# Kernel tuning notes

Hardware: AMD Instinct MI355X
Metric: run time of the kernel (lower is better)

The kernel has to match this reference:

```python
import jax, jax.numpy as jnp
import numpy as np

L, B, T, D = 4, 2, 1024, 2048
HQ, HKV, DK = 16, 4, 128
HID = 5464
CAND = 896


def setup_inputs() -> dict:
    key = jax.random.key(0)
    ks = jax.random.split(key, 8)
    s = lambda fan: fan ** -0.5
    return {
        "x": jax.random.normal(ks[0], (B, T, D), jnp.float32),
        "s1": jnp.ones((L, D), jnp.float32),
        "s2": jnp.ones((L, D), jnp.float32),
        "s3": jnp.ones((L, D), jnp.float32),
        "wq": jax.random.normal(ks[1], (L, D, HQ * DK), jnp.float32) * s(D),
        "wk": jax.random.normal(ks[2], (L, D, HKV * DK), jnp.float32) * s(D),
        "wv": jax.random.normal(ks[3], (L, D, HKV * DK), jnp.float32) * s(D),
        "wo": jax.random.normal(ks[4], (L, HQ * DK, D), jnp.float32) * s(HQ * DK),
        "w_gate": jax.random.normal(ks[5], (L, D, HID), jnp.float32) * s(D),
        "w_val": jax.random.normal(ks[6], (L, D, HID), jnp.float32) * s(D),
        "w_out": jax.random.normal(ks[7], (L, HID, D), jnp.float32) * s(HID),
        "cand_offset": CAND,
    }


def _rmsnorm(x, scale, eps=1e-5):
    xf = x.astype(jnp.float32)
    n = xf * jax.lax.rsqrt(jnp.mean(xf * xf, axis=-1, keepdims=True) + eps)
    return (scale * n).astype(x.dtype)


def _rope_cos_sin(t_len, dk):
    inv = 1.0 / (10000.0 ** (jnp.arange(0, dk, 2, dtype=jnp.float32) / dk))
    fr = jnp.outer(jnp.arange(t_len, dtype=jnp.float32), inv)
    emb = jnp.concatenate([fr, fr], axis=-1)  # [T, dk]
    return jnp.cos(emb)[None, :, None, :], jnp.sin(emb)[None, :, None, :]


def _rotate_half(x):
    x1, x2 = jnp.split(x, 2, axis=-1)
    return jnp.concatenate([-x2, x1], axis=-1)


def reference(x, s1, s2, s3, wq, wk, wv, wo, w_gate, w_val, w_out, cand_offset):
    Bsz, Tlen, _ = x.shape
    # recsys mask: causal history; candidates attend to history + self only
    r = jnp.arange(Tlen)[:, None]
    c = jnp.arange(Tlen)[None, :]
    mask = (c <= r) & ~((r >= cand_offset) & (c >= cand_offset) & (r != c))  # [T,T] bool
    cos, sin = _rope_cos_sin(Tlen, DK)
    nrep = HQ // HKV
    h = x
    for l in range(wq.shape[0]):
        hn = _rmsnorm(h, s1[l])
        q = (hn @ wq[l]).reshape(Bsz, Tlen, HQ, DK)
        k = (hn @ wk[l]).reshape(Bsz, Tlen, HKV, DK)
        v = (hn @ wv[l]).reshape(Bsz, Tlen, HKV, DK)
        q = q * cos + _rotate_half(q) * sin
        k = k * cos + _rotate_half(k) * sin
        k = jnp.repeat(k, nrep, axis=2)  # GQA expand -> [B,T,HQ,DK]
        v = jnp.repeat(v, nrep, axis=2)
        logits = jnp.einsum('bthd,bshd->bhts', q, k)  # attn_output_multiplier = 1.0
        logits = jnp.where(mask[None, None], logits, -jnp.inf)
        attn = jax.nn.softmax(logits.astype(jnp.float32), axis=-1).astype(x.dtype)
        o = jnp.einsum('bhts,bshd->bthd', attn, v).reshape(Bsz, Tlen, HQ * DK)
        h = h + o @ wo[l]
        hn = _rmsnorm(h, s2[l])
        ff = (jax.nn.gelu(hn @ w_gate[l], approximate=False) * (hn @ w_val[l])) @ w_out[l]
        h = h + ff
        h = _rmsnorm(h, s3[l])
    return h
```

## Files before the change

### kernel.cpp

```cpp
#include <hip/hip_runtime.h>
#include <stdint.h>

#define L_ 4
#define B_ 2
#define T_ 1024
#define D_ 2048
#define HQ_ 16
#define HKV_ 4
#define DK_ 128
#define HID_ 5464
#define HIDP_ 5504
#define BT_ (B_*T_)
#define NQKV_ (HQ_*DK_ + 2*HKV_*DK_)
#define VOFF_ (HQ_*DK_ + HKV_*DK_)

typedef unsigned short u16;
typedef float f32x4 __attribute__((ext_vector_type(4)));
typedef __bf16 bf16x8 __attribute__((ext_vector_type(8)));

__device__ __forceinline__ u16 f2bs(float f) {
  unsigned u = __float_as_uint(f);
  u += 0x7fffu + ((u >> 16) & 1u);
  return (u16)(u >> 16);
}
__device__ __forceinline__ float bs2f(u16 s) {
  return __uint_as_float(((unsigned)s) << 16);
}

__device__ __forceinline__ void async16(void* lds, const void* g) {
  __builtin_amdgcn_global_load_lds(
      (const __attribute__((address_space(1))) unsigned*)(uintptr_t)g,
      (__attribute__((address_space(3))) unsigned*)(unsigned)(uintptr_t)lds,
      16, 0, 0);
}

__device__ __forceinline__ f32x4 mfma16(bf16x8 a, bf16x8 b, f32x4 c) {
  return __builtin_amdgcn_mfma_f32_16x16x32_bf16(a, b, c, 0, 0, 0);
}

__device__ __forceinline__ void remap_bid(int& bm, int& bn) {
  const int nbx = gridDim.x, nby = gridDim.y;
  const int nwg = nbx * nby;
  const int lin = blockIdx.y * nbx + blockIdx.x;
  const int q = nwg >> 3, r = nwg & 7;
  const int xcd = lin & 7, rest = lin >> 3;
  const int wgid = (xcd < r ? xcd * (q + 1) : r * (q + 1) + (xcd - r) * q) + rest;
  const int GROUP = 4;
  const int tpg = GROUP * nby;
  const int gid = wgid / tpg;
  const int first = gid * GROUP;
  const int size = (GROUP < nbx - first) ? GROUP : (nbx - first);
  const int rem = wgid - gid * tpg;
  bn = first + rem % size;
  bm = rem / size;
}

__global__ void copy_f4_k(const float4* __restrict__ src, float4* __restrict__ dst, int n4) {
  int i = blockIdx.x * blockDim.x + threadIdx.x;
  if (i < n4) dst[i] = src[i];
}

__global__ void rope_tab_k(float* __restrict__ ct, float* __restrict__ st) {
  int idx = blockIdx.x * 256 + threadIdx.x;
  int t = idx >> 6, i = idx & 63;
  float inv = expf(-(float)i * (9.210340371976184f / 64.f));
  float fr = (float)t * inv;
  ct[idx] = cosf(fr);
  st[idx] = sinf(fr);
}

__global__ __launch_bounds__(256) void cvt_split_s_k(const float* __restrict__ in,
    uint2* __restrict__ ohi, uint2* __restrict__ olo, int S, int C, int n4) {
  int i = blockIdx.x * 256 + threadIdx.x;
  if (i >= n4) return;
  const int r4 = C >> 2;
  const int row = i / r4, c4 = i - row * r4;
  float4 v = *(const float4*)(in + (size_t)row * S + c4 * 4);
  u16 h0 = f2bs(v.x), h1 = f2bs(v.y), h2 = f2bs(v.z), h3 = f2bs(v.w);
  u16 l0 = f2bs(v.x - bs2f(h0)), l1 = f2bs(v.y - bs2f(h1));
  u16 l2 = f2bs(v.z - bs2f(h2)), l3 = f2bs(v.w - bs2f(h3));
  uint2 ph, pl;
  ph.x = (unsigned)h0 | ((unsigned)h1 << 16); ph.y = (unsigned)h2 | ((unsigned)h3 << 16);
  pl.x = (unsigned)l0 | ((unsigned)l1 << 16); pl.y = (unsigned)l2 | ((unsigned)l3 << 16);
  ohi[i] = ph; olo[i] = pl;
}

__global__ __launch_bounds__(256) void transpose_split_k(
    const float* __restrict__ in, u16* __restrict__ outh, u16* __restrict__ outl,
    int inR, int inC, int outC) {
  __shared__ float tile[64][65];
  const int oj0 = blockIdx.x * 64;
  const int oi0 = blockIdx.y * 64;
  #pragma unroll
  for (int rep = 0; rep < 16; ++rep) {
    int idx = rep * 256 + threadIdx.x;
    int a = idx >> 6, b = idx & 63;
    int ir = oj0 + a, ic = oi0 + b;
    tile[a][b] = (ir < inR && ic < inC) ? in[(size_t)ir * inC + ic] : 0.f;
  }
  __syncthreads();
  #pragma unroll
  for (int rep = 0; rep < 16; ++rep) {
    int idx = rep * 256 + threadIdx.x;
    int ii = idx >> 6, jj = idx & 63;
    float val = tile[jj][ii];
    u16 hh = f2bs(val);
    const size_t o = (size_t)(oi0 + ii) * outC + oj0 + jj;
    outh[o] = hh;
    outl[o] = f2bs(val - bs2f(hh));
  }
}

__global__ __launch_bounds__(256) void transpose_v_split_k(const float* __restrict__ qkv,
    u16* __restrict__ vth, u16* __restrict__ vtl) {
  __shared__ float tile[64][65];
  const int bz = blockIdx.z;
  const int b = bz >> 2, hkv = bz & 3;
  const int t0 = blockIdx.x * 64, d0 = blockIdx.y * 64;
  #pragma unroll
  for (int rep = 0; rep < 16; ++rep) {
    int idx = rep * 256 + threadIdx.x;
    int a = idx >> 6, c = idx & 63;
    tile[a][c] = qkv[(size_t)(b * T_ + t0 + a) * NQKV_ + VOFF_ + hkv * DK_ + d0 + c];
  }
  __syncthreads();
  #pragma unroll
  for (int rep = 0; rep < 16; ++rep) {
    int idx = rep * 256 + threadIdx.x;
    int aa = idx & 63, cc = idx >> 6;
    float val = tile[aa][cc];
    u16 hh = f2bs(val);
    const size_t o = ((size_t)bz * DK_ + d0 + cc) * T_ + t0 + aa;
    vth[o] = hh;
    vtl[o] = f2bs(val - bs2f(hh));
  }
}

__global__ __launch_bounds__(256) void rmsnorm_f(const float* x,
    const float* __restrict__ sc, float* out) {
  const int row = blockIdx.x;
  const float* xr = x + (size_t)row * D_;
  float ss = 0.f;
  #pragma unroll
  for (int it = 0; it < D_ / 1024; ++it) {
    int i = (it * 256 + threadIdx.x) * 4;
    float4 v = *(const float4*)(xr + i);
    ss += v.x * v.x + v.y * v.y + v.z * v.z + v.w * v.w;
  }
  #pragma unroll
  for (int o = 1; o < 64; o <<= 1) ss += __shfl_xor(ss, o);
  __shared__ float red[4];
  if ((threadIdx.x & 63) == 0) red[threadIdx.x >> 6] = ss;
  __syncthreads();
  float tot = red[0] + red[1] + red[2] + red[3];
  float r = rsqrtf(tot * (1.f / D_) + 1e-5f);
  float* orow = out + (size_t)row * D_;
  #pragma unroll
  for (int it = 0; it < D_ / 1024; ++it) {
    int i = (it * 256 + threadIdx.x) * 4;
    float4 v = *(const float4*)(xr + i);
    float4 s4 = *(const float4*)(sc + i);
    float4 o4;
    o4.x = v.x * s4.x * r; o4.y = v.y * s4.y * r;
    o4.z = v.z * s4.z * r; o4.w = v.w * s4.w * r;
    *(float4*)(orow + i) = o4;
  }
}

__global__ __launch_bounds__(256) void rmsnorm_s(const float* x,
    const float* __restrict__ sc, u16* ohi, u16* olo) {
  const int row = blockIdx.x;
  const float* xr = x + (size_t)row * D_;
  float ss = 0.f;
  #pragma unroll
  for (int it = 0; it < D_ / 1024; ++it) {
    int i = (it * 256 + threadIdx.x) * 4;
    float4 v = *(const float4*)(xr + i);
    ss += v.x * v.x + v.y * v.y + v.z * v.z + v.w * v.w;
  }
  #pragma unroll
  for (int o = 1; o < 64; o <<= 1) ss += __shfl_xor(ss, o);
  __shared__ float red[4];
  if ((threadIdx.x & 63) == 0) red[threadIdx.x >> 6] = ss;
  __syncthreads();
  float tot = red[0] + red[1] + red[2] + red[3];
  float r = rsqrtf(tot * (1.f / D_) + 1e-5f);
  #pragma unroll
  for (int it = 0; it < D_ / 1024; ++it) {
    int i = (it * 256 + threadIdx.x) * 4;
    float4 v = *(const float4*)(xr + i);
    float4 s4 = *(const float4*)(sc + i);
    float o0 = v.x * s4.x * r, o1 = v.y * s4.y * r, o2 = v.z * s4.z * r, o3 = v.w * s4.w * r;
    u16 h0 = f2bs(o0), h1 = f2bs(o1), h2 = f2bs(o2), h3 = f2bs(o3);
    u16 l0 = f2bs(o0 - bs2f(h0)), l1 = f2bs(o1 - bs2f(h1));
    u16 l2 = f2bs(o2 - bs2f(h2)), l3 = f2bs(o3 - bs2f(h3));
    uint2 ph, pl;
    ph.x = (unsigned)h0 | ((unsigned)h1 << 16); ph.y = (unsigned)h2 | ((unsigned)h3 << 16);
    pl.x = (unsigned)l0 | ((unsigned)l1 << 16); pl.y = (unsigned)l2 | ((unsigned)l3 << 16);
    *(uint2*)(ohi + (size_t)row * D_ + i) = ph;
    *(uint2*)(olo + (size_t)row * D_ + i) = pl;
  }
}

template <int MODE>
__global__ __launch_bounds__(512, 4) void gemm_bts_k(
    const u16* __restrict__ Ahi, const u16* __restrict__ Alo,
    const u16* __restrict__ Bthi, const u16* __restrict__ Btlo,
    float* Cf, u16* Chi, u16* Clo, int N, int K) {
  __shared__ u16 smem[128 * 32 * 4 * 2];
  const int tid = threadIdx.x, w = tid >> 6, lane = tid & 63;
  const int g = lane >> 4, r16 = lane & 15;
  int bm, bn;
  remap_bid(bm, bn);
  const int m0 = bm * 128, n0 = bn * 128;
  const int wr = w >> 1, wc = w & 1;
  f32x4 acc[2][4] = {};
  const int nkt = K >> 5;

  const int sp = tid * 16;
  const int srow = sp >> 6;
  const int ssc = ((sp >> 4) & 3) ^ ((srow >> 1) & 3);
  auto stage = [&](int kt, int buf) {
    char* base = (char*)smem + buf * 32768;
    const size_t ga = (size_t)(m0 + srow) * K + (kt << 5) + ssc * 8;
    const size_t gb = (size_t)(n0 + srow) * K + (kt << 5) + ssc * 8;
    async16(base + sp, Ahi + ga);
    async16(base + 8192 + sp, Alo + ga);
    async16(base + 16384 + sp, Bthi + gb);
    async16(base + 24576 + sp, Btlo + gb);
  };

  stage(0, 0);
  for (int kt = 0; kt < nkt; ++kt) {
    const int cur = kt & 1;
    if (kt + 1 < nkt) {
      stage(kt + 1, cur ^ 1);
      asm volatile("s_waitcnt vmcnt(4)" ::: "memory");
    } else {
      asm volatile("s_waitcnt vmcnt(0)" ::: "memory");
    }
    __builtin_amdgcn_s_barrier();
    __builtin_amdgcn_sched_barrier(0);
    char* Ash = (char*)smem + cur * 32768;
    char* Asl = Ash + 8192;
    char* Bsh = Ash + 16384;
    char* Bsl = Ash + 24576;
    bf16x8 ah[2], al[2], bh[4], bl[4];
    #pragma unroll
    for (int m = 0; m < 2; ++m) {
      const int row = wr * 32 + m * 16 + r16;
      const int ch = g ^ ((row >> 1) & 3);
      const int off = row * 64 + ch * 16;
      ah[m] = *(const bf16x8*)(Ash + off);
      al[m] = *(const bf16x8*)(Asl + off);
    }
    #pragma unroll
    for (int n = 0; n < 4; ++n) {
      const int row = wc * 64 + n * 16 + r16;
      const int ch = g ^ ((row >> 1) & 3);
      const int off = row * 64 + ch * 16;
      bh[n] = *(const bf16x8*)(Bsh + off);
      bl[n] = *(const bf16x8*)(Bsl + off);
    }
    #pragma unroll
    for (int m = 0; m < 2; ++m)
      #pragma unroll
      for (int n = 0; n < 4; ++n) {
        acc[m][n] = mfma16(ah[m], bh[n], acc[m][n]);
        acc[m][n] = mfma16(ah[m], bl[n], acc[m][n]);
        acc[m][n] = mfma16(al[m], bh[n], acc[m][n]);
      }
    asm volatile("s_waitcnt lgkmcnt(0)" ::: "memory");
    __builtin_amdgcn_s_barrier();
    __builtin_amdgcn_sched_barrier(0);
  }
  #pragma unroll
  for (int m = 0; m < 2; ++m) {
    const int rbase = m0 + wr * 32 + m * 16 + g * 4;
    #pragma unroll
    for (int n = 0; n < 4; ++n) {
      const int c = n0 + wc * 64 + n * 16 + r16;
      #pragma unroll
      for (int j = 0; j < 4; ++j) {
        const size_t idx = (size_t)(rbase + j) * N + c;
        const float v = acc[m][n][j];
        if constexpr (MODE == 0) {
          Cf[idx] = v;
        } else if constexpr (MODE == 1) {
          Cf[idx] += v;
        } else if constexpr (MODE == 2) {
          const float gv = bs2f(Chi[idx]) + bs2f(Clo[idx]);
          const float ge = 0.5f * gv * (1.f + erff(gv * 0.70710678118654752f));
          const float r = ge * v;
          const u16 rh = f2bs(r);
          Chi[idx] = rh;
          Clo[idx] = f2bs(r - bs2f(rh));
        } else {
          const u16 rh = f2bs(v);
          Chi[idx] = rh;
          Clo[idx] = f2bs(v - bs2f(rh));
        }
      }
    }
  }
}

__global__ __launch_bounds__(256) void rope_qkv_k(float* qkv,
    const float* __restrict__ ct, const float* __restrict__ st) {
  const int row = blockIdx.x;
  const int t = row & (T_ - 1);
  float* src = qkv + (size_t)row * NQKV_;
  for (int idx = threadIdx.x; idx < HQ_ * 64; idx += 256) {
    int h = idx >> 6, i = idx & 63;
    float c = ct[t * 64 + i], s = st[t * 64 + i];
    float x1 = src[h * DK_ + i], x2 = src[h * DK_ + i + 64];
    src[h * DK_ + i]      = x1 * c - x2 * s;
    src[h * DK_ + i + 64] = x2 * c + x1 * s;
  }
  float* kr = src + HQ_ * DK_;
  for (int idx = threadIdx.x; idx < HKV_ * 64; idx += 256) {
    int h = idx >> 6, i = idx & 63;
    float c = ct[t * 64 + i], s = st[t * 64 + i];
    float x1 = kr[h * DK_ + i], x2 = kr[h * DK_ + i + 64];
    kr[h * DK_ + i]      = x1 * c - x2 * s;
    kr[h * DK_ + i + 64] = x2 * c + x1 * s;
  }
}

__global__ __launch_bounds__(256) void attn_s_k(
    const u16* __restrict__ Qh, const u16* __restrict__ Ql,
    const u16* __restrict__ Kh, const u16* __restrict__ Kl,
    const u16* __restrict__ VTh, const u16* __restrict__ VTl,
    u16* __restrict__ Ohi, u16* __restrict__ Olo, const int* __restrict__ candp) {
  __shared__ u16 sm[40960];
  char* Kth = (char*)sm;
  char* Ktl = (char*)sm + 16384;
  char* Vth = (char*)sm + 32768;
  char* Vtl = (char*)sm + 49152;
  const int b = blockIdx.z, hq = blockIdx.y, q0 = blockIdx.x * 64;
  const int hkv = hq >> 2;
  const int tid = threadIdx.x, w = tid >> 6, lane = tid & 63;
  const int g = lane >> 4, r16 = lane & 15;
  char* Pth = (char*)sm + 65536 + w * 2048;
  char* Ptl = (char*)sm + 65536 + 8192 + w * 2048;
  const int CANDv = *candp;
  const int qrow = q0 + w * 16 + r16;
  const int pmask = (r16 & 7) << 4;
  const u16* qph = Qh + ((size_t)(b * T_ + qrow) * HQ_ + hq) * DK_;
  const u16* qpl = Ql + ((size_t)(b * T_ + qrow) * HQ_ + hq) * DK_;
  bf16x8 qh[4], ql[4];
  #pragma unroll
  for (int ks = 0; ks < 4; ++ks) {
    qh[ks] = *(const bf16x8*)(qph + ks * 32 + g * 8);
    ql[ks] = *(const bf16x8*)(qpl + ks * 32 + g * 8);
  }

  float m_run = -1e30f, l_run = 0.f;
  f32x4 oacc[8] = {};

  const int ntile = blockIdx.x + 1;
  for (int it = 0; it < ntile; ++it) {
    const int c0 = it * 64;
    if (c0 >= CANDv && c0 + 63 < q0) continue;
    #pragma unroll
    for (int inst = 0; inst < 4; ++inst) {
      const int p = (inst * 4 + w) * 1024 + lane * 16;
      const int rowK = p >> 8;
      const int scK = ((p >> 4) & 15) ^ (rowK & 7);
      const size_t gk = ((size_t)(b * T_ + c0 + rowK) * HKV_ + hkv) * DK_ + scK * 8;
      async16(Kth + p, Kh + gk);
      async16(Ktl + p, Kl + gk);
      const int rowV = p >> 7;
      const int scV = ((p >> 4) & 7) ^ (rowV & 7);
      const size_t gv = ((size_t)(b * HKV_ + hkv) * DK_ + rowV) * T_ + c0 + scV * 8;
      async16(Vth + p, VTh + gv);
      async16(Vtl + p, VTl + gv);
    }
    asm volatile("s_waitcnt vmcnt(0)" ::: "memory");
    __syncthreads();

    f32x4 stf[4] = {};
    #pragma unroll
    for (int ks = 0; ks < 4; ++ks) {
      #pragma unroll
      for (int kf = 0; kf < 4; ++kf) {
        const int row = kf * 16 + r16;
        const int ch = (ks * 4 + g) ^ (row & 7);
        const int off = row * 256 + ch * 16;
        bf16x8 akh = *(const bf16x8*)(Kth + off);
        bf16x8 akl = *(const bf16x8*)(Ktl + off);
        stf[kf] = mfma16(akh, qh[ks], stf[kf]);
        stf[kf] = mfma16(akh, ql[ks], stf[kf]);
        stf[kf] = mfma16(akl, qh[ks], stf[kf]);
      }
    }
    float pv[16];
    float tmax = -1e30f;
    #pragma unroll
    for (int kf = 0; kf < 4; ++kf)
      #pragma unroll
      for (int j = 0; j < 4; ++j) {
        const int c = c0 + kf * 16 + g * 4 + j;
        float s = stf[kf][j];
        const bool ok = (c <= qrow) && !((qrow >= CANDv) && (c >= CANDv) && (c != qrow));
        s = ok ? s : -1e30f;
        pv[kf * 4 + j] = s;
        tmax = fmaxf(tmax, s);
      }
    tmax = fmaxf(tmax, __shfl_xor(tmax, 16));
    tmax = fmaxf(tmax, __shfl_xor(tmax, 32));
    const float mnew = fmaxf(m_run, tmax);
    const float scal = __expf(m_run - mnew);
    float psum = 0.f;
    #pragma unroll
    for (int i = 0; i < 16; ++i) {
      const float e = (pv[i] > -1e29f) ? __expf(pv[i] - mnew) : 0.f;
      pv[i] = e; psum += e;
    }
    psum += __shfl_xor(psum, 16);
    psum += __shfl_xor(psum, 32);
    l_run = l_run * scal + psum;
    m_run = mnew;
    #pragma unroll
    for (int df = 0; df < 8; ++df)
      #pragma unroll
      for (int j = 0; j < 4; ++j) oacc[df][j] *= scal;
    #pragma unroll
    for (int kf = 0; kf < 4; ++kf) {
      u16 h0 = f2bs(pv[kf * 4 + 0]), h1 = f2bs(pv[kf * 4 + 1]);
      u16 h2 = f2bs(pv[kf * 4 + 2]), h3 = f2bs(pv[kf * 4 + 3]);
      u16 l0 = f2bs(pv[kf * 4 + 0] - bs2f(h0)), l1 = f2bs(pv[kf * 4 + 1] - bs2f(h1));
      u16 l2 = f2bs(pv[kf * 4 + 2] - bs2f(h2)), l3 = f2bs(pv[kf * 4 + 3] - bs2f(h3));
      uint2 ph, pl;
      ph.x = (unsigned)h0 | ((unsigned)h1 << 16); ph.y = (unsigned)h2 | ((unsigned)h3 << 16);
      pl.x = (unsigned)l0 | ((unsigned)l1 << 16); pl.y = (unsigned)l2 | ((unsigned)l3 << 16);
      *(uint2*)(Pth + r16 * 128 + ((kf * 32 + g * 8) ^ pmask)) = ph;
      *(uint2*)(Ptl + r16 * 128 + ((kf * 32 + g * 8) ^ pmask)) = pl;
    }
    asm volatile("s_waitcnt lgkmcnt(0)" ::: "memory");
    __builtin_amdgcn_sched_barrier(0);
    #pragma unroll
    for (int ks = 0; ks < 2; ++ks) {
      bf16x8 pfh = *(const bf16x8*)(Pth + r16 * 128 + ((ks * 64 + g * 16) ^ pmask));
      bf16x8 pfl = *(const bf16x8*)(Ptl + r16 * 128 + ((ks * 64 + g * 16) ^ pmask));
      #pragma unroll
      for (int df = 0; df < 8; ++df) {
        const int row = df * 16 + r16;
        const int ch = (ks * 4 + g) ^ (row & 7);
        const int off = row * 128 + ch * 16;
        bf16x8 avh = *(const bf16x8*)(Vth + off);
        bf16x8 avl = *(const bf16x8*)(Vtl + off);
        oacc[df] = mfma16(avh, pfh, oacc[df]);
        oacc[df] = mfma16(avh, pfl, oacc[df]);
        oacc[df] = mfma16(avl, pfh, oacc[df]);
      }
    }
    __syncthreads();
  }
  const float inv = 1.f / l_run;
  u16* oph = Ohi + ((size_t)(b * T_ + qrow) * HQ_ + hq) * DK_;
  u16* opl = Olo + ((size_t)(b * T_ + qrow) * HQ_ + hq) * DK_;
  #pragma unroll
  for (int df = 0; df < 8; ++df) {
    float o0 = oacc[df][0] * inv, o1 = oacc[df][1] * inv;
    float o2 = oacc[df][2] * inv, o3 = oacc[df][3] * inv;
    u16 h0 = f2bs(o0), h1 = f2bs(o1), h2 = f2bs(o2), h3 = f2bs(o3);
    u16 l0 = f2bs(o0 - bs2f(h0)), l1 = f2bs(o1 - bs2f(h1));
    u16 l2 = f2bs(o2 - bs2f(h2)), l3 = f2bs(o3 - bs2f(h3));
    uint2 ph, pl;
    ph.x = (unsigned)h0 | ((unsigned)h1 << 16); ph.y = (unsigned)h2 | ((unsigned)h3 << 16);
    pl.x = (unsigned)l0 | ((unsigned)l1 << 16); pl.y = (unsigned)l2 | ((unsigned)l3 << 16);
    *(uint2*)(oph + df * 16 + g * 4) = ph;
    *(uint2*)(opl + df * 16 + g * 4) = pl;
  }
}

extern "C" void kernel_launch(void* const* d_in, const int* in_sizes, int n_in,
                              void* d_out, int out_size, void* d_ws, size_t ws_size,
                              hipStream_t stream) {
  (void)in_sizes; (void)n_in; (void)out_size; (void)ws_size;
  const float* x    = (const float*)d_in[0];
  const float* s1   = (const float*)d_in[1];
  const float* s2   = (const float*)d_in[2];
  const float* s3   = (const float*)d_in[3];
  const float* wq   = (const float*)d_in[4];
  const float* wk   = (const float*)d_in[5];
  const float* wv   = (const float*)d_in[6];
  const float* wo   = (const float*)d_in[7];
  const float* wg   = (const float*)d_in[8];
  const float* wvl  = (const float*)d_in[9];
  const float* wout = (const float*)d_in[10];
  const int*   cand = (const int*)d_in[11];

  float* h = (float*)d_out;
  char* ws = (char*)d_ws;
  size_t off = 0;
  auto nxt = [&](size_t bytes) -> char* {
    char* p = ws + off; off += (bytes + 255) & ~(size_t)255; return p;
  };
  u16* wThi  = (u16*)nxt((size_t)HIDP_ * D_ * 2);
  u16* wTlo  = (u16*)nxt((size_t)HIDP_ * D_ * 2);
  u16* hnhi  = (u16*)nxt((size_t)BT_ * D_ * 2);
  u16* hnlo  = (u16*)nxt((size_t)BT_ * D_ * 2);
  char* U    = nxt((size_t)68 << 20);
  float* ct  = (float*)nxt((size_t)T_ * 64 * 4);
  float* st  = (float*)nxt((size_t)T_ * 64 * 4);
  size_t uo = 0;
  auto unxt = [&](size_t bytes) -> char* {
    char* p = U + uo; uo += (bytes + 255) & ~(size_t)255; return p;
  };
  float* qkvf = (float*)unxt((size_t)BT_ * NQKV_ * 4);
  u16* qbhi   = (u16*)unxt((size_t)BT_ * HQ_ * DK_ * 2);
  u16* qblo   = (u16*)unxt((size_t)BT_ * HQ_ * DK_ * 2);
  u16* kbhi   = (u16*)unxt((size_t)BT_ * HKV_ * DK_ * 2);
  u16* kblo   = (u16*)unxt((size_t)BT_ * HKV_ * DK_ * 2);
  u16* vthi   = (u16*)unxt((size_t)BT_ * HKV_ * DK_ * 2);
  u16* vtlo   = (u16*)unxt((size_t)BT_ * HKV_ * DK_ * 2);
  u16* obhi   = (u16*)unxt((size_t)BT_ * HQ_ * DK_ * 2);
  u16* oblo   = (u16*)unxt((size_t)BT_ * HQ_ * DK_ * 2);
  u16* ghi = (u16*)U;
  u16* glo = (u16*)(U + (size_t)BT_ * HIDP_ * 2);

  copy_f4_k<<<BT_ * D_ / 4 / 256, 256, 0, stream>>>((const float4*)x, (float4*)h, BT_ * D_ / 4);
  rope_tab_k<<<T_ * 64 / 256, 256, 0, stream>>>(ct, st);

  for (int l = 0; l < L_; ++l) {
    const float* wq_l   = wq   + (size_t)l * D_ * (HQ_ * DK_);
    const float* wk_l   = wk   + (size_t)l * D_ * (HKV_ * DK_);
    const float* wv_l   = wv   + (size_t)l * D_ * (HKV_ * DK_);
    const float* wo_l   = wo   + (size_t)l * (HQ_ * DK_) * D_;
    const float* wg_l   = wg   + (size_t)l * D_ * HID_;
    const float* wvl_l  = wvl  + (size_t)l * D_ * HID_;
    const float* wout_l = wout + (size_t)l * HID_ * D_;

    rmsnorm_s<<<BT_, 256, 0, stream>>>(h, s1 + (size_t)l * D_, hnhi, hnlo);
    transpose_split_k<<<dim3(32, 32), 256, 0, stream>>>(wq_l, wThi, wTlo, D_, HQ_ * DK_, D_);
    transpose_split_k<<<dim3(32, 8), 256, 0, stream>>>(wk_l, wThi + (size_t)HQ_ * DK_ * D_,
        wTlo + (size_t)HQ_ * DK_ * D_, D_, HKV_ * DK_, D_);
    transpose_split_k<<<dim3(32, 8), 256, 0, stream>>>(wv_l, wThi + (size_t)VOFF_ * D_,
        wTlo + (size_t)VOFF_ * D_, D_, HKV_ * DK_, D_);
    gemm_bts_k<0><<<dim3(NQKV_ / 128, BT_ / 128), 512, 0, stream>>>(
        hnhi, hnlo, wThi, wTlo, qkvf, nullptr, nullptr, NQKV_, D_);
    rope_qkv_k<<<BT_, 256, 0, stream>>>(qkvf, ct, st);
    cvt_split_s_k<<<BT_ * D_ / 4 / 256, 256, 0, stream>>>(qkvf,
        (uint2*)qbhi, (uint2*)qblo, NQKV_, HQ_ * DK_, BT_ * HQ_ * DK_ / 4);
    cvt_split_s_k<<<BT_ * HKV_ * DK_ / 4 / 256, 256, 0, stream>>>(qkvf + HQ_ * DK_,
        (uint2*)kbhi, (uint2*)kblo, NQKV_, HKV_ * DK_, BT_ * HKV_ * DK_ / 4);
    transpose_v_split_k<<<dim3(T_ / 64, DK_ / 64, B_ * HKV_), 256, 0, stream>>>(qkvf, vthi, vtlo);
    attn_s_k<<<dim3(T_ / 64, HQ_, B_), 256, 0, stream>>>(
        qbhi, qblo, kbhi, kblo, vthi, vtlo, obhi, oblo, cand);
    transpose_split_k<<<dim3(32, 32), 256, 0, stream>>>(wo_l, wThi, wTlo, HQ_ * DK_, D_, D_);
    gemm_bts_k<1><<<dim3(D_ / 128, BT_ / 128), 512, 0, stream>>>(
        obhi, oblo, wThi, wTlo, h, nullptr, nullptr, D_, D_);

    rmsnorm_s<<<BT_, 256, 0, stream>>>(h, s2 + (size_t)l * D_, hnhi, hnlo);
    transpose_split_k<<<dim3(32, HIDP_ / 64), 256, 0, stream>>>(wg_l, wThi, wTlo, D_, HID_, D_);
    gemm_bts_k<3><<<dim3(HIDP_ / 128, BT_ / 128), 512, 0, stream>>>(
        hnhi, hnlo, wThi, wTlo, nullptr, ghi, glo, HIDP_, D_);
    transpose_split_k<<<dim3(32, HIDP_ / 64), 256, 0, stream>>>(wvl_l, wThi, wTlo, D_, HID_, D_);
    gemm_bts_k<2><<<dim3(HIDP_ / 128, BT_ / 128), 512, 0, stream>>>(
        hnhi, hnlo, wThi, wTlo, nullptr, ghi, glo, HIDP_, D_);
    transpose_split_k<<<dim3(HIDP_ / 64, 32), 256, 0, stream>>>(wout_l, wThi, wTlo, HID_, D_, HIDP_);
    gemm_bts_k<1><<<dim3(D_ / 128, BT_ / 128), 512, 0, stream>>>(
        ghi, glo, wThi, wTlo, h, nullptr, nullptr, D_, HIDP_);
    rmsnorm_f<<<BT_, 256, 0, stream>>>(h, s3 + (size_t)l * D_, h);
  }
}
```

Before: 3.205 ms.

## Fuse RoPE with bf16 split and single-buffer the GEMM staging

Merges the RoPE kernel and the two fp32-to-bf16 hi/lo split kernels into one pass that writes the split Q and K buffers directly. This drops two launches and one read-write round trip of the QKV buffer. Separately, the GEMM drops double buffering: it uses a single 32KB LDS stage with a full vmcnt(0) wait and __syncthreads each k-step, and raises launch bounds to 8 waves per EU. The aim is higher occupancy, at the cost of no longer overlapping global loads with the MFMA work inside a block.

Measured after the change: 8.936 ms. 179% more time.

```diff
diff --git a/kernel.cpp b/kernel.cpp
--- a/kernel.cpp
+++ b/kernel.cpp
@@ -69,22 +69,6 @@
   st[idx] = sinf(fr);
 }
 
-__global__ __launch_bounds__(256) void cvt_split_s_k(const float* __restrict__ in,
-    uint2* __restrict__ ohi, uint2* __restrict__ olo, int S, int C, int n4) {
-  int i = blockIdx.x * 256 + threadIdx.x;
-  if (i >= n4) return;
-  const int r4 = C >> 2;
-  const int row = i / r4, c4 = i - row * r4;
-  float4 v = *(const float4*)(in + (size_t)row * S + c4 * 4);
-  u16 h0 = f2bs(v.x), h1 = f2bs(v.y), h2 = f2bs(v.z), h3 = f2bs(v.w);
-  u16 l0 = f2bs(v.x - bs2f(h0)), l1 = f2bs(v.y - bs2f(h1));
-  u16 l2 = f2bs(v.z - bs2f(h2)), l3 = f2bs(v.w - bs2f(h3));
-  uint2 ph, pl;
-  ph.x = (unsigned)h0 | ((unsigned)h1 << 16); ph.y = (unsigned)h2 | ((unsigned)h3 << 16);
-  pl.x = (unsigned)l0 | ((unsigned)l1 << 16); pl.y = (unsigned)l2 | ((unsigned)l3 << 16);
-  ohi[i] = ph; olo[i] = pl;
-}
-
 __global__ __launch_bounds__(256) void transpose_split_k(
     const float* __restrict__ in, u16* __restrict__ outh, u16* __restrict__ outl,
     int inR, int inC, int outC) {
@@ -203,11 +187,11 @@
 }
 
 template <int MODE>
-__global__ __launch_bounds__(512, 4) void gemm_bts_k(
+__global__ __launch_bounds__(512, 8) void gemm_bts_k(
     const u16* __restrict__ Ahi, const u16* __restrict__ Alo,
     const u16* __restrict__ Bthi, const u16* __restrict__ Btlo,
     float* Cf, u16* Chi, u16* Clo, int N, int K) {
-  __shared__ u16 smem[128 * 32 * 4 * 2];
+  __shared__ u16 smem[128 * 32 * 4];
   const int tid = threadIdx.x, w = tid >> 6, lane = tid & 63;
   const int g = lane >> 4, r16 = lane & 15;
   int bm, bn;
@@ -220,31 +204,22 @@
   const int sp = tid * 16;
   const int srow = sp >> 6;
   const int ssc = ((sp >> 4) & 3) ^ ((srow >> 1) & 3);
-  auto stage = [&](int kt, int buf) {
-    char* base = (char*)smem + buf * 32768;
-    const size_t ga = (size_t)(m0 + srow) * K + (kt << 5) + ssc * 8;
-    const size_t gb = (size_t)(n0 + srow) * K + (kt << 5) + ssc * 8;
-    async16(base + sp, Ahi + ga);
-    async16(base + 8192 + sp, Alo + ga);
-    async16(base + 16384 + sp, Bthi + gb);
-    async16(base + 24576 + sp, Btlo + gb);
-  };
-
-  stage(0, 0);
+  char* Ash = (char*)smem;
+  char* Asl = (char*)smem + 8192;
+  char* Bsh = (char*)smem + 16384;
+  char* Bsl = (char*)smem + 24576;
+
   for (int kt = 0; kt < nkt; ++kt) {
-    const int cur = kt & 1;
-    if (kt + 1 < nkt) {
-      stage(kt + 1, cur ^ 1);
-      asm volatile("s_waitcnt vmcnt(4)" ::: "memory");
-    } else {
-      asm volatile("s_waitcnt vmcnt(0)" ::: "memory");
-    }
-    __builtin_amdgcn_s_barrier();
-    __builtin_amdgcn_sched_barrier(0);
-    char* Ash = (char*)smem + cur * 32768;
-    char* Asl = Ash + 8192;
-    char* Bsh = Ash + 16384;
-    char* Bsl = Ash + 24576;
+    {
+      const size_t ga = (size_t)(m0 + srow) * K + (kt << 5) + ssc * 8;
+      const size_t gb = (size_t)(n0 + srow) * K + (kt << 5) + ssc * 8;
+      async16(Ash + sp, Ahi + ga);
+      async16(Asl + sp, Alo + ga);
+      async16(Bsh + sp, Bthi + gb);
+      async16(Bsl + sp, Btlo + gb);
+    }
+    asm volatile("s_waitcnt vmcnt(0)" ::: "memory");
+    __syncthreads();
     bf16x8 ah[2], al[2], bh[4], bl[4];
     #pragma unroll
     for (int m = 0; m < 2; ++m) {
@@ -270,9 +245,7 @@
         acc[m][n] = mfma16(ah[m], bl[n], acc[m][n]);
         acc[m][n] = mfma16(al[m], bh[n], acc[m][n]);
       }
-    asm volatile("s_waitcnt lgkmcnt(0)" ::: "memory");
-    __builtin_amdgcn_s_barrier();
-    __builtin_amdgcn_sched_barrier(0);
+    __syncthreads();
   }
   #pragma unroll
   for (int m = 0; m < 2; ++m) {
@@ -305,25 +278,37 @@
   }
 }
 
-__global__ __launch_bounds__(256) void rope_qkv_k(float* qkv,
-    const float* __restrict__ ct, const float* __restrict__ st) {
+__global__ __launch_bounds__(256) void rope_split_qkv_k(const float* __restrict__ qkv,
+    const float* __restrict__ ct, const float* __restrict__ st,
+    u16* __restrict__ qhi, u16* __restrict__ qlo,
+    u16* __restrict__ khi, u16* __restrict__ klo) {
   const int row = blockIdx.x;
   const int t = row & (T_ - 1);
-  float* src = qkv + (size_t)row * NQKV_;
+  const float* src = qkv + (size_t)row * NQKV_;
+  u16* qh = qhi + (size_t)row * (HQ_ * DK_);
+  u16* ql = qlo + (size_t)row * (HQ_ * DK_);
   for (int idx = threadIdx.x; idx < HQ_ * 64; idx += 256) {
     int h = idx >> 6, i = idx & 63;
     float c = ct[t * 64 + i], s = st[t * 64 + i];
     float x1 = src[h * DK_ + i], x2 = src[h * DK_ + i + 64];
-    src[h * DK_ + i]      = x1 * c - x2 * s;
-    src[h * DK_ + i + 64] = x2 * c + x1 * s;
-  }
-  float* kr = src + HQ_ * DK_;
+    float r1 = x1 * c - x2 * s;
+    float r2 = x2 * c + x1 * s;
+    u16 h1 = f2bs(r1), h2v = f2bs(r2);
+    qh[h * DK_ + i]      = h1;  ql[h * DK_ + i]      = f2bs(r1 - bs2f(h1));
+    qh[h * DK_ + i + 64] = h2v; ql[h * DK_ + i + 64] = f2bs(r2 - bs2f(h2v));
+  }
+  const float* srck = src + HQ_ * DK_;
+  u16* kh = khi + (size_t)row * (HKV_ * DK_);
+  u16* kl = klo + (size_t)row * (HKV_ * DK_);
   for (int idx = threadIdx.x; idx < HKV_ * 64; idx += 256) {
     int h = idx >> 6, i = idx & 63;
     float c = ct[t * 64 + i], s = st[t * 64 + i];
-    float x1 = kr[h * DK_ + i], x2 = kr[h * DK_ + i + 64];
-    kr[h * DK_ + i]      = x1 * c - x2 * s;
-    kr[h * DK_ + i + 64] = x2 * c + x1 * s;
+    float x1 = srck[h * DK_ + i], x2 = srck[h * DK_ + i + 64];
+    float r1 = x1 * c - x2 * s;
+    float r2 = x2 * c + x1 * s;
+    u16 h1 = f2bs(r1), h2v = f2bs(r2);
+    kh[h * DK_ + i]      = h1;  kl[h * DK_ + i]      = f2bs(r1 - bs2f(h1));
+    kh[h * DK_ + i + 64] = h2v; kl[h * DK_ + i + 64] = f2bs(r2 - bs2f(h2v));
   }
 }
 
@@ -541,11 +526,7 @@
         wTlo + (size_t)VOFF_ * D_, D_, HKV_ * DK_, D_);
     gemm_bts_k<0><<<dim3(NQKV_ / 128, BT_ / 128), 512, 0, stream>>>(
         hnhi, hnlo, wThi, wTlo, qkvf, nullptr, nullptr, NQKV_, D_);
-    rope_qkv_k<<<BT_, 256, 0, stream>>>(qkvf, ct, st);
-    cvt_split_s_k<<<BT_ * D_ / 4 / 256, 256, 0, stream>>>(qkvf,
-        (uint2*)qbhi, (uint2*)qblo, NQKV_, HQ_ * DK_, BT_ * HQ_ * DK_ / 4);
-    cvt_split_s_k<<<BT_ * HKV_ * DK_ / 4 / 256, 256, 0, stream>>>(qkvf + HQ_ * DK_,
-        (uint2*)kbhi, (uint2*)kblo, NQKV_, HKV_ * DK_, BT_ * HKV_ * DK_ / 4);
+    rope_split_qkv_k<<<BT_, 256, 0, stream>>>(qkvf, ct, st, qbhi, qblo, kbhi, kblo);
     transpose_v_split_k<<<dim3(T_ / 64, DK_ / 64, B_ * HKV_), 256, 0, stream>>>(qkvf, vthi, vtlo);
     attn_s_k<<<dim3(T_ / 64, HQ_, B_), 256, 0, stream>>>(
         qbhi, qblo, kbhi, kblo, vthi, vtlo, obhi, oblo, cand);
```
